# Optimization experiments

Measured on AMD Instinct MI355X. Metric: run time of the kernel, lower is better.

Reference implementation:

```python
import jax, jax.numpy as jnp
import numpy as np

EMB = 1024
B, N = 4, 2048


def setup_inputs() -> dict:
    key = jax.random.key(0)
    ks = jax.random.split(key, 10)
    s = 1.0 / np.sqrt(EMB)
    return {
        "x": jax.random.normal(ks[0], (B, N, EMB), dtype=jnp.float32),
        "Wq": jax.random.normal(ks[1], (EMB, EMB), dtype=jnp.float32) * s,
        "bq": jnp.zeros((EMB,), dtype=jnp.float32),
        "Wk": jax.random.normal(ks[2], (EMB, EMB), dtype=jnp.float32) * s,
        "bk": jnp.zeros((EMB,), dtype=jnp.float32),
        "Wv": jax.random.normal(ks[3], (EMB, EMB), dtype=jnp.float32) * s,
        "bv": jnp.zeros((EMB,), dtype=jnp.float32),
        "Wm": jax.random.normal(ks[4], (EMB, EMB), dtype=jnp.float32) * s,
        "bm": jnp.zeros((EMB,), dtype=jnp.float32),
    }


def reference(x, Wq, bq, Wk, bk, Wv, bv, Wm, bm):
    # Projections (torch Linear: x @ W^T + b; here W is stored pre-transposed)
    q = x @ Wq + bq  # [B,N,D]
    k = x @ Wk + bk
    v = x @ Wv + bv
    # scores[b,i,j] = q[b,i,:] . k[b,j,:]  (no 1/sqrt(d) scaling in original)
    scores = jnp.einsum("bid,bjd->bij", q, k)
    # NOTE: softmax over dim=1 (the query/i axis), as in the original
    alpha = jax.nn.softmax(scores, axis=1)  # [B,N,N]
    # t[b,j,d] = sum_i v[b,i,d] * alpha[b,i,j]  == alpha^T @ v per batch
    t = jnp.einsum("bij,bid->bjd", alpha, v)  # [B,N,D]
    # MLP(emb, emb, []) is a single Linear, followed by outer relu
    return jax.nn.relu(t @ Wm + bm)
```

## Files before the change

kernel.cpp:

```cpp
#include <hip/hip_runtime.h>
#include <hip/hip_bf16.h>
#include <hip/hip_fp16.h>
#include <math.h>

#define EMB 1024
#define SEQ 2048
#define BATCH 4

typedef _Float16 half8 __attribute__((ext_vector_type(8)));
typedef float floatx4 __attribute__((ext_vector_type(4)));

__device__ __forceinline__ void gload_lds16(const void* g, void* l) {
    __builtin_amdgcn_global_load_lds(
        (const __attribute__((address_space(1))) void*)g,
        (__attribute__((address_space(3))) void*)l, 16, 0, 0);
}

__device__ __forceinline__ void pipe_sync() {
    asm volatile("s_waitcnt vmcnt(0)" ::: "memory");
    __builtin_amdgcn_s_barrier();
    __builtin_amdgcn_sched_barrier(0);
}

template <int EPI>
__global__ __launch_bounds__(256) void gemm_bt(
    const _Float16* __restrict__ A, const _Float16* __restrict__ B,
    void* __restrict__ Cv, const float* __restrict__ bias,
    int M, int N, int K, long sAb, long sBb, long sCb) {
    __shared__ _Float16 As0[128 * 32];
    __shared__ _Float16 Bs0[128 * 32];
    __shared__ _Float16 As1[128 * 32];
    __shared__ _Float16 Bs1[128 * 32];
    const int tid = threadIdx.x;
    const int lane = tid & 63;
    const int wave = tid >> 6;
    const long zb = blockIdx.z;
    A += zb * sAb;
    B += zb * sBb;
    const int bm = blockIdx.x * 128;
    const int bn = blockIdx.y * 128;
    floatx4 acc[4][4];
#pragma unroll
    for (int mi = 0; mi < 4; ++mi)
#pragma unroll
        for (int ni = 0; ni < 4; ++ni) acc[mi][ni] = (floatx4){0.f, 0.f, 0.f, 0.f};

    const int srow = lane >> 2;
    const int scol = (lane & 3) * 8;
    const int wm = (wave >> 1) * 64;
    const int wn = (wave & 1) * 64;
    const int fr = lane & 15;
    const int fk = (lane >> 4) * 8;

#define STAGE(AS, BS, kt)                                                      \
    {                                                                          \
        _Pragma("unroll") for (int c = 0; c < 2; ++c) {                        \
            const int rr = wave * 32 + c * 16 + srow;                          \
            gload_lds16(A + (long)(bm + rr) * K + (kt) + scol,                 \
                        &AS[(wave * 2 + c) * 512]);                            \
            gload_lds16(B + (long)(bn + rr) * K + (kt) + scol,                 \
                        &BS[(wave * 2 + c) * 512]);                            \
        }                                                                      \
    }

#define COMPUTE(AS, BS)                                                        \
    {                                                                          \
        half8 af[4], bf[4];                                                    \
        _Pragma("unroll") for (int mi = 0; mi < 4; ++mi)                       \
            af[mi] = *(const half8*)&AS[(wm + mi * 16 + fr) * 32 + fk];        \
        _Pragma("unroll") for (int ni = 0; ni < 4; ++ni)                       \
            bf[ni] = *(const half8*)&BS[(wn + ni * 16 + fr) * 32 + fk];        \
        _Pragma("unroll") for (int mi = 0; mi < 4; ++mi)                       \
            _Pragma("unroll") for (int ni = 0; ni < 4; ++ni)                   \
                acc[mi][ni] = __builtin_amdgcn_mfma_f32_16x16x32_f16(          \
                    af[mi], bf[ni], acc[mi][ni], 0, 0, 0);                     \
    }

    const int T = K >> 5;
    STAGE(As0, Bs0, 0);
    pipe_sync();
    for (int t = 0; t < T; t += 2) {
        STAGE(As1, Bs1, (t + 1) << 5);
        COMPUTE(As0, Bs0);
        pipe_sync();
        if (t + 2 < T) STAGE(As0, Bs0, (t + 2) << 5);
        COMPUTE(As1, Bs1);
        pipe_sync();
    }
#undef STAGE
#undef COMPUTE

    const int er = (lane >> 4) * 4;
    const int ec = lane & 15;
#pragma unroll
    for (int mi = 0; mi < 4; ++mi) {
#pragma unroll
        for (int ni = 0; ni < 4; ++ni) {
            const int col = bn + wn + ni * 16 + ec;
#pragma unroll
            for (int r = 0; r < 4; ++r) {
                const int row = bm + wm + mi * 16 + er + r;
                float v = acc[mi][ni][r];
                if (EPI == 0 || EPI == 1 || EPI == 3) v += bias[col];
                if (EPI == 3) v = fmaxf(v, 0.f);
                if (EPI == 0 || EPI == 4) {
                    ((_Float16*)Cv)[zb * sCb + (long)row * N + col] = (_Float16)v;
                } else if (EPI == 1) {
                    const long b = row >> 11;
                    const long i = row & (SEQ - 1);
                    ((_Float16*)Cv)[(b * EMB + col) * SEQ + i] = (_Float16)v;
                } else {
                    ((float*)Cv)[zb * sCb + (long)row * N + col] = v;
                }
            }
        }
    }
}

__global__ __launch_bounds__(256) void softmax_rows(const float* __restrict__ P,
                                                    _Float16* __restrict__ Aout) {
    const long row = blockIdx.x;
    const float* p = P + row * (long)SEQ;
    const int tid = threadIdx.x;
    float4 x0 = ((const float4*)p)[2 * tid];
    float4 x1 = ((const float4*)p)[2 * tid + 1];
    float v[8] = {x0.x, x0.y, x0.z, x0.w, x1.x, x1.y, x1.z, x1.w};
    float m = v[0];
#pragma unroll
    for (int j = 1; j < 8; ++j) m = fmaxf(m, v[j]);
#pragma unroll
    for (int o = 32; o; o >>= 1) m = fmaxf(m, __shfl_xor(m, o));
    __shared__ float rbuf[4];
    __shared__ float sbuf[4];
    const int lane = tid & 63, wv = tid >> 6;
    if (!lane) rbuf[wv] = m;
    __syncthreads();
    m = fmaxf(fmaxf(rbuf[0], rbuf[1]), fmaxf(rbuf[2], rbuf[3]));
    float s = 0.f;
#pragma unroll
    for (int j = 0; j < 8; ++j) {
        v[j] = expf(v[j] - m);
        s += v[j];
    }
#pragma unroll
    for (int o = 32; o; o >>= 1) s += __shfl_xor(s, o);
    if (!lane) sbuf[wv] = s;
    __syncthreads();
    s = sbuf[0] + sbuf[1] + sbuf[2] + sbuf[3];
    const float inv = 1.f / s;
    half8 h;
#pragma unroll
    for (int j = 0; j < 8; ++j) h[j] = (_Float16)(v[j] * inv);
    *(half8*)(Aout + row * (long)SEQ + tid * 8) = h;
}

__global__ __launch_bounds__(256) void cast_x(const float* __restrict__ X,
                                              _Float16* __restrict__ Xh) {
    const long i = (long)(blockIdx.x * 256 + threadIdx.x) * 8;
    float4 a = ((const float4*)(X + i))[0];
    float4 b = ((const float4*)(X + i))[1];
    half8 h;
    h[0] = (_Float16)a.x; h[1] = (_Float16)a.y; h[2] = (_Float16)a.z; h[3] = (_Float16)a.w;
    h[4] = (_Float16)b.x; h[5] = (_Float16)b.y; h[6] = (_Float16)b.z; h[7] = (_Float16)b.w;
    *(half8*)(Xh + i) = h;
}

__global__ __launch_bounds__(256) void transpose_cast(const float* __restrict__ W,
                                                      _Float16* __restrict__ Wt) {
    __shared__ float tile[32][33];
    const int bx = blockIdx.x * 32;
    const int by = blockIdx.y * 32;
    const int tx = threadIdx.x, ty = threadIdx.y;
#pragma unroll
    for (int r = 0; r < 32; r += 8)
        tile[ty + r][tx] = W[(long)(by + ty + r) * EMB + bx + tx];
    __syncthreads();
#pragma unroll
    for (int r = 0; r < 32; r += 8)
        Wt[(long)(bx + ty + r) * EMB + by + tx] = (_Float16)tile[tx][ty + r];
}

extern "C" void kernel_launch(void* const* d_in, const int* in_sizes, int n_in,
                              void* d_out, int out_size, void* d_ws, size_t ws_size,
                              hipStream_t stream) {
    const float* x  = (const float*)d_in[0];
    const float* Wq = (const float*)d_in[1];
    const float* bq = (const float*)d_in[2];
    const float* Wk = (const float*)d_in[3];
    const float* bk = (const float*)d_in[4];
    const float* Wv = (const float*)d_in[5];
    const float* bv = (const float*)d_in[6];
    const float* Wm = (const float*)d_in[7];
    const float* bm = (const float*)d_in[8];
    float* out = (float*)d_out;

    char* ws = (char*)d_ws;
    const long MB = 1l << 20;
    _Float16* xh  = (_Float16*)(ws + 0 * MB);
    _Float16* wqt = (_Float16*)(ws + 16 * MB);
    _Float16* wkt = (_Float16*)(ws + 18 * MB);
    _Float16* wvt = (_Float16*)(ws + 20 * MB);
    _Float16* wmt = (_Float16*)(ws + 22 * MB);
    _Float16* q   = (_Float16*)(ws + 24 * MB);
    _Float16* k   = (_Float16*)(ws + 40 * MB);
    _Float16* vt  = (_Float16*)(ws + 56 * MB);
    _Float16* t   = (_Float16*)(ws + 72 * MB);
    float*    P   = (float*)(ws + 88 * MB);
    _Float16* al  = (_Float16*)(ws + 152 * MB);

    const long MN = (long)BATCH * SEQ;

    cast_x<<<4096, 256, 0, stream>>>(x, xh);
    transpose_cast<<<dim3(32, 32), dim3(32, 8), 0, stream>>>(Wq, wqt);
    transpose_cast<<<dim3(32, 32), dim3(32, 8), 0, stream>>>(Wk, wkt);
    transpose_cast<<<dim3(32, 32), dim3(32, 8), 0, stream>>>(Wv, wvt);
    transpose_cast<<<dim3(32, 32), dim3(32, 8), 0, stream>>>(Wm, wmt);

    gemm_bt<0><<<dim3(64, 8), 256, 0, stream>>>(xh, wqt, q, bq, (int)MN, EMB, EMB, 0, 0, 0);
    gemm_bt<0><<<dim3(64, 8), 256, 0, stream>>>(xh, wkt, k, bk, (int)MN, EMB, EMB, 0, 0, 0);
    gemm_bt<1><<<dim3(64, 8), 256, 0, stream>>>(xh, wvt, vt, bv, (int)MN, EMB, EMB, 0, 0, 0);

    gemm_bt<2><<<dim3(16, 16, BATCH), 256, 0, stream>>>(
        k, q, P, nullptr, SEQ, SEQ, EMB,
        (long)SEQ * EMB, (long)SEQ * EMB, (long)SEQ * SEQ);

    softmax_rows<<<BATCH * SEQ, 256, 0, stream>>>(P, al);

    gemm_bt<4><<<dim3(16, 8, BATCH), 256, 0, stream>>>(
        al, vt, t, nullptr, SEQ, EMB, SEQ,
        (long)SEQ * SEQ, (long)EMB * SEQ, (long)SEQ * EMB);

    gemm_bt<3><<<dim3(64, 8), 256, 0, stream>>>(t, wmt, out, bm, (int)MN, EMB, EMB, 0, 0, 0);
}
```

Measured before the change: 350.9 us.

## Use 256x128 tiles with 512 threads and a 4-stage LDS prefetch pipeline

Replaces the double-buffered 128x128 GEMM kernel with one using 512 threads, 256x128 block tiles and a 4-deep ring of LDS buffers. Three k-tiles are kept in flight, and partial vmcnt waits let later loads overlap the current MFMA work instead of draining all loads every step. Grid sizes are halved along M to match. The larger tile reuses each B tile more and hides memory latency better, at the cost of more LDS per block (96KB), which lowers occupancy, and fewer blocks for the smaller GEMMs.

```diff
diff --git a/kernel.cpp b/kernel.cpp
--- a/kernel.cpp
+++ b/kernel.cpp
@@ -16,28 +16,39 @@
         (__attribute__((address_space(3))) void*)l, 16, 0, 0);
 }
 
-__device__ __forceinline__ void pipe_sync() {
+__device__ __forceinline__ void bar_cnt6() {
+    __builtin_amdgcn_sched_barrier(0);
+    asm volatile("s_waitcnt vmcnt(6)" ::: "memory");
+    __builtin_amdgcn_s_barrier();
+    __builtin_amdgcn_sched_barrier(0);
+}
+__device__ __forceinline__ void bar_cnt3() {
+    __builtin_amdgcn_sched_barrier(0);
+    asm volatile("s_waitcnt vmcnt(3)" ::: "memory");
+    __builtin_amdgcn_s_barrier();
+    __builtin_amdgcn_sched_barrier(0);
+}
+__device__ __forceinline__ void bar_cnt0() {
+    __builtin_amdgcn_sched_barrier(0);
     asm volatile("s_waitcnt vmcnt(0)" ::: "memory");
     __builtin_amdgcn_s_barrier();
     __builtin_amdgcn_sched_barrier(0);
 }
 
 template <int EPI>
-__global__ __launch_bounds__(256) void gemm_bt(
+__global__ __launch_bounds__(512) void gemm_p(
     const _Float16* __restrict__ A, const _Float16* __restrict__ B,
     void* __restrict__ Cv, const float* __restrict__ bias,
     int M, int N, int K, long sAb, long sBb, long sCb) {
-    __shared__ _Float16 As0[128 * 32];
-    __shared__ _Float16 Bs0[128 * 32];
-    __shared__ _Float16 As1[128 * 32];
-    __shared__ _Float16 Bs1[128 * 32];
+    __shared__ _Float16 As[4][256 * 32];
+    __shared__ _Float16 Bs[4][128 * 32];
     const int tid = threadIdx.x;
     const int lane = tid & 63;
     const int wave = tid >> 6;
     const long zb = blockIdx.z;
     A += zb * sAb;
     B += zb * sBb;
-    const int bm = blockIdx.x * 128;
+    const int bm = blockIdx.x * 256;
     const int bn = blockIdx.y * 128;
     floatx4 acc[4][4];
 #pragma unroll
@@ -45,48 +56,54 @@
 #pragma unroll
         for (int ni = 0; ni < 4; ++ni) acc[mi][ni] = (floatx4){0.f, 0.f, 0.f, 0.f};
 
-    const int srow = lane >> 2;
-    const int scol = (lane & 3) * 8;
+    const int srow = tid >> 2;
+    const int scol = (tid & 3) * 8;
+    const long ag0 = (long)(bm + srow) * K + scol;
+    const long ag1 = (long)(bm + 128 + srow) * K + scol;
+    const long bg0 = (long)(bn + srow) * K + scol;
     const int wm = (wave >> 1) * 64;
     const int wn = (wave & 1) * 64;
     const int fr = lane & 15;
     const int fk = (lane >> 4) * 8;
 
-#define STAGE(AS, BS, kt)                                                      \
+#define STAGE(t_)                                                              \
     {                                                                          \
-        _Pragma("unroll") for (int c = 0; c < 2; ++c) {                        \
-            const int rr = wave * 32 + c * 16 + srow;                          \
-            gload_lds16(A + (long)(bm + rr) * K + (kt) + scol,                 \
-                        &AS[(wave * 2 + c) * 512]);                            \
-            gload_lds16(B + (long)(bn + rr) * K + (kt) + scol,                 \
-                        &BS[(wave * 2 + c) * 512]);                            \
-        }                                                                      \
-    }
-
-#define COMPUTE(AS, BS)                                                        \
+        const int b_ = (t_) & 3;                                               \
+        const int kt_ = (t_) * 32;                                             \
+        gload_lds16(A + ag0 + kt_, &As[b_][wave * 512]);                       \
+        gload_lds16(A + ag1 + kt_, &As[b_][4096 + wave * 512]);                \
+        gload_lds16(B + bg0 + kt_, &Bs[b_][wave * 512]);                       \
+    }
+
+#define COMPUTE(t_)                                                            \
     {                                                                          \
+        const int b_ = (t_) & 3;                                               \
         half8 af[4], bf[4];                                                    \
         _Pragma("unroll") for (int mi = 0; mi < 4; ++mi)                       \
-            af[mi] = *(const half8*)&AS[(wm + mi * 16 + fr) * 32 + fk];        \
+            af[mi] = *(const half8*)&As[b_][(wm + mi * 16 + fr) * 32 + fk];    \
         _Pragma("unroll") for (int ni = 0; ni < 4; ++ni)                       \
-            bf[ni] = *(const half8*)&BS[(wn + ni * 16 + fr) * 32 + fk];        \
+            bf[ni] = *(const half8*)&Bs[b_][(wn + ni * 16 + fr) * 32 + fk];    \
         _Pragma("unroll") for (int mi = 0; mi < 4; ++mi)                       \
             _Pragma("unroll") for (int ni = 0; ni < 4; ++ni)                   \
                 acc[mi][ni] = __builtin_amdgcn_mfma_f32_16x16x32_f16(          \
                     af[mi], bf[ni], acc[mi][ni], 0, 0, 0);                     \
     }
 
-    const int T = K >> 5;
-    STAGE(As0, Bs0, 0);
-    pipe_sync();
-    for (int t = 0; t < T; t += 2) {
-        STAGE(As1, Bs1, (t + 1) << 5);
-        COMPUTE(As0, Bs0);
-        pipe_sync();
-        if (t + 2 < T) STAGE(As0, Bs0, (t + 2) << 5);
-        COMPUTE(As1, Bs1);
-        pipe_sync();
-    }
+    const int NT = K >> 5;
+    STAGE(0);
+    STAGE(1);
+    STAGE(2);
+    bar_cnt6();
+    for (int t = 0; t < NT - 3; ++t) {
+        STAGE(t + 3);
+        COMPUTE(t);
+        bar_cnt6();
+    }
+    COMPUTE(NT - 3);
+    bar_cnt3();
+    COMPUTE(NT - 2);
+    bar_cnt0();
+    COMPUTE(NT - 1);
 #undef STAGE
 #undef COMPUTE
 
@@ -216,19 +233,19 @@
     transpose_cast<<<dim3(32, 32), dim3(32, 8), 0, stream>>>(Wv, wvt);
     transpose_cast<<<dim3(32, 32), dim3(32, 8), 0, stream>>>(Wm, wmt);
 
-    gemm_bt<0><<<dim3(64, 8), 256, 0, stream>>>(xh, wqt, q, bq, (int)MN, EMB, EMB, 0, 0, 0);
-    gemm_bt<0><<<dim3(64, 8), 256, 0, stream>>>(xh, wkt, k, bk, (int)MN, EMB, EMB, 0, 0, 0);
-    gemm_bt<1><<<dim3(64, 8), 256, 0, stream>>>(xh, wvt, vt, bv, (int)MN, EMB, EMB, 0, 0, 0);
-
-    gemm_bt<2><<<dim3(16, 16, BATCH), 256, 0, stream>>>(
+    gemm_p<0><<<dim3(32, 8), 512, 0, stream>>>(xh, wqt, q, bq, (int)MN, EMB, EMB, 0, 0, 0);
+    gemm_p<0><<<dim3(32, 8), 512, 0, stream>>>(xh, wkt, k, bk, (int)MN, EMB, EMB, 0, 0, 0);
+    gemm_p<1><<<dim3(32, 8), 512, 0, stream>>>(xh, wvt, vt, bv, (int)MN, EMB, EMB, 0, 0, 0);
+
+    gemm_p<2><<<dim3(8, 16, BATCH), 512, 0, stream>>>(
         k, q, P, nullptr, SEQ, SEQ, EMB,
         (long)SEQ * EMB, (long)SEQ * EMB, (long)SEQ * SEQ);
 
     softmax_rows<<<BATCH * SEQ, 256, 0, stream>>>(P, al);
 
-    gemm_bt<4><<<dim3(16, 8, BATCH), 256, 0, stream>>>(
+    gemm_p<4><<<dim3(8, 8, BATCH), 512, 0, stream>>>(
         al, vt, t, nullptr, SEQ, EMB, SEQ,
         (long)SEQ * SEQ, (long)EMB * SEQ, (long)SEQ * EMB);
 
-    gemm_bt<3><<<dim3(64, 8), 256, 0, stream>>>(t, wmt, out, bm, (int)MN, EMB, EMB, 0, 0, 0);
-}
+    gemm_p<3><<<dim3(32, 8), 512, 0, stream>>>(t, wmt, out, bm, (int)MN, EMB, EMB, 0, 0, 0);
+}
```

Result: slower. 373.3 us (+6.4%).

## Rewrite GEMM as 8-wave 256x128 tile with triple-buffered swizzled LDS pipeline

Applied to the files above, without the earlier changes.

The GEMM kernel moves from 4 waves on a 128x128 tile with BK=32 double buffering to 8 waves on a 256x128 tile with BK=64. LDS is triple-buffered and uses XOR-swizzled layouts to avoid bank conflicts. The loop is split into two phases per tile that interleave global-to-LDS loads with MFMA, using partial vmcnt waits and raised wave priority during compute. This aims to hide memory latency and raise MFMA utilization, at the cost of about 144KB of LDS per block (which limits occupancy) and fewer blocks per grid.

```diff
diff --git a/kernel.cpp b/kernel.cpp
--- a/kernel.cpp
+++ b/kernel.cpp
@@ -16,28 +16,25 @@
         (__attribute__((address_space(3))) void*)l, 16, 0, 0);
 }
 
-__device__ __forceinline__ void pipe_sync() {
-    asm volatile("s_waitcnt vmcnt(0)" ::: "memory");
+__device__ __forceinline__ void sbar() {
+    __builtin_amdgcn_sched_barrier(0);
     __builtin_amdgcn_s_barrier();
     __builtin_amdgcn_sched_barrier(0);
 }
 
 template <int EPI>
-__global__ __launch_bounds__(256) void gemm_bt(
+__global__ __launch_bounds__(512) void gemm_8p(
     const _Float16* __restrict__ A, const _Float16* __restrict__ B,
     void* __restrict__ Cv, const float* __restrict__ bias,
     int M, int N, int K, long sAb, long sBb, long sCb) {
-    __shared__ _Float16 As0[128 * 32];
-    __shared__ _Float16 Bs0[128 * 32];
-    __shared__ _Float16 As1[128 * 32];
-    __shared__ _Float16 Bs1[128 * 32];
+    __shared__ _Float16 lds[3 * 24576];
     const int tid = threadIdx.x;
     const int lane = tid & 63;
     const int wave = tid >> 6;
     const long zb = blockIdx.z;
     A += zb * sAb;
     B += zb * sBb;
-    const int bm = blockIdx.x * 128;
+    const int bm = blockIdx.x * 256;
     const int bn = blockIdx.y * 128;
     floatx4 acc[4][4];
 #pragma unroll
@@ -45,50 +42,85 @@
 #pragma unroll
         for (int ni = 0; ni < 4; ++ni) acc[mi][ni] = (floatx4){0.f, 0.f, 0.f, 0.f};
 
-    const int srow = lane >> 2;
-    const int scol = (lane & 3) * 8;
+    const int srow = tid >> 3;
+    const int ssl = (tid & 7) ^ (srow & 7);
+    const _Float16* Ag = A + (long)(bm + srow) * K + ssl * 8;
+    const _Float16* Bg = B + (long)(bn + srow) * K + ssl * 8;
+    const long K64 = (long)K * 64;
+    const int ldst = wave * 512;
+
     const int wm = (wave >> 1) * 64;
     const int wn = (wave & 1) * 64;
-    const int fr = lane & 15;
-    const int fk = (lane >> 4) * 8;
-
-#define STAGE(AS, BS, kt)                                                      \
-    {                                                                          \
-        _Pragma("unroll") for (int c = 0; c < 2; ++c) {                        \
-            const int rr = wave * 32 + c * 16 + srow;                          \
-            gload_lds16(A + (long)(bm + rr) * K + (kt) + scol,                 \
-                        &AS[(wave * 2 + c) * 512]);                            \
-            gload_lds16(B + (long)(bn + rr) * K + (kt) + scol,                 \
-                        &BS[(wave * 2 + c) * 512]);                            \
-        }                                                                      \
-    }
-
-#define COMPUTE(AS, BS)                                                        \
+    const int l15 = lane & 15;
+    const int x7 = lane & 7;
+    const int g4 = lane >> 4;
+    const int sl0 = (g4 ^ x7) * 8;
+    const int sl1 = ((4 + g4) ^ x7) * 8;
+    const int fA0 = (wm + l15) * 64 + sl0;
+    const int fA1 = (wm + l15) * 64 + sl1;
+    const int fB0 = 16384 + (wn + l15) * 64 + sl0;
+    const int fB1 = 16384 + (wn + l15) * 64 + sl1;
+
+#define STG_H0(kt_, so_)                                                       \
+    gload_lds16(Ag + (kt_), &lds[(so_) + ldst]);                               \
+    gload_lds16(Ag + K64 + (kt_), &lds[(so_) + 4096 + ldst]);                  \
+    gload_lds16(Bg + (kt_), &lds[(so_) + 16384 + ldst]);
+#define STG_H1(kt_, so_)                                                       \
+    gload_lds16(Ag + 2 * K64 + (kt_), &lds[(so_) + 8192 + ldst]);              \
+    gload_lds16(Ag + 3 * K64 + (kt_), &lds[(so_) + 12288 + ldst]);             \
+    gload_lds16(Bg + K64 + (kt_), &lds[(so_) + 16384 + 4096 + ldst]);
+
+#define PHASE(fa_, fb_, co_, STG_)                                             \
     {                                                                          \
         half8 af[4], bf[4];                                                    \
         _Pragma("unroll") for (int mi = 0; mi < 4; ++mi)                       \
-            af[mi] = *(const half8*)&AS[(wm + mi * 16 + fr) * 32 + fk];        \
+            af[mi] = *(const half8*)&lds[(co_) + (fa_) + mi * 1024];           \
         _Pragma("unroll") for (int ni = 0; ni < 4; ++ni)                       \
-            bf[ni] = *(const half8*)&BS[(wn + ni * 16 + fr) * 32 + fk];        \
+            bf[ni] = *(const half8*)&lds[(co_) + (fb_) + ni * 1024];           \
+        STG_                                                                   \
+        sbar();                                                                \
+        asm volatile("s_waitcnt lgkmcnt(0)" ::: "memory");                     \
+        __builtin_amdgcn_sched_barrier(0);                                     \
+        __builtin_amdgcn_s_setprio(1);                                         \
         _Pragma("unroll") for (int mi = 0; mi < 4; ++mi)                       \
             _Pragma("unroll") for (int ni = 0; ni < 4; ++ni)                   \
                 acc[mi][ni] = __builtin_amdgcn_mfma_f32_16x16x32_f16(          \
                     af[mi], bf[ni], acc[mi][ni], 0, 0, 0);                     \
-    }
-
-    const int T = K >> 5;
-    STAGE(As0, Bs0, 0);
-    pipe_sync();
-    for (int t = 0; t < T; t += 2) {
-        STAGE(As1, Bs1, (t + 1) << 5);
-        COMPUTE(As0, Bs0);
-        pipe_sync();
-        if (t + 2 < T) STAGE(As0, Bs0, (t + 2) << 5);
-        COMPUTE(As1, Bs1);
-        pipe_sync();
-    }
-#undef STAGE
-#undef COMPUTE
+        __builtin_amdgcn_s_setprio(0);                                         \
+    }
+
+#define TILE_END(n_)                                                           \
+    __builtin_amdgcn_sched_barrier(0);                                         \
+    asm volatile("s_waitcnt vmcnt(" #n_ ")" ::: "memory");                     \
+    __builtin_amdgcn_s_barrier();                                              \
+    __builtin_amdgcn_sched_barrier(0);
+
+    STG_H0(0, 0) STG_H1(0, 0)
+    STG_H0(64, 24576) STG_H1(64, 24576)
+    TILE_END(6)
+    int co = 0, so = 49152;
+    const int NT = K >> 6;
+    for (int t = 0; t < NT - 2; ++t) {
+        const long kt2 = (long)(t + 2) << 6;
+        PHASE(fA0, fB0, co, STG_H0(kt2, so))
+        sbar();
+        PHASE(fA1, fB1, co, STG_H1(kt2, so))
+        TILE_END(6)
+        co += 24576; if (co == 73728) co = 0;
+        so += 24576; if (so == 73728) so = 0;
+    }
+    PHASE(fA0, fB0, co, )
+    sbar();
+    PHASE(fA1, fB1, co, )
+    TILE_END(0)
+    co += 24576; if (co == 73728) co = 0;
+    PHASE(fA0, fB0, co, )
+    sbar();
+    PHASE(fA1, fB1, co, )
+#undef STG_H0
+#undef STG_H1
+#undef PHASE
+#undef TILE_END
 
     const int er = (lane >> 4) * 4;
     const int ec = lane & 15;
@@ -216,19 +248,19 @@
     transpose_cast<<<dim3(32, 32), dim3(32, 8), 0, stream>>>(Wv, wvt);
     transpose_cast<<<dim3(32, 32), dim3(32, 8), 0, stream>>>(Wm, wmt);
 
-    gemm_bt<0><<<dim3(64, 8), 256, 0, stream>>>(xh, wqt, q, bq, (int)MN, EMB, EMB, 0, 0, 0);
-    gemm_bt<0><<<dim3(64, 8), 256, 0, stream>>>(xh, wkt, k, bk, (int)MN, EMB, EMB, 0, 0, 0);
-    gemm_bt<1><<<dim3(64, 8), 256, 0, stream>>>(xh, wvt, vt, bv, (int)MN, EMB, EMB, 0, 0, 0);
-
-    gemm_bt<2><<<dim3(16, 16, BATCH), 256, 0, stream>>>(
+    gemm_8p<0><<<dim3(32, 8), 512, 0, stream>>>(xh, wqt, q, bq, (int)MN, EMB, EMB, 0, 0, 0);
+    gemm_8p<0><<<dim3(32, 8), 512, 0, stream>>>(xh, wkt, k, bk, (int)MN, EMB, EMB, 0, 0, 0);
+    gemm_8p<1><<<dim3(32, 8), 512, 0, stream>>>(xh, wvt, vt, bv, (int)MN, EMB, EMB, 0, 0, 0);
+
+    gemm_8p<2><<<dim3(8, 16, BATCH), 512, 0, stream>>>(
         k, q, P, nullptr, SEQ, SEQ, EMB,
         (long)SEQ * EMB, (long)SEQ * EMB, (long)SEQ * SEQ);
 
     softmax_rows<<<BATCH * SEQ, 256, 0, stream>>>(P, al);
 
-    gemm_bt<4><<<dim3(16, 8, BATCH), 256, 0, stream>>>(
+    gemm_8p<4><<<dim3(8, 8, BATCH), 512, 0, stream>>>(
         al, vt, t, nullptr, SEQ, EMB, SEQ,
         (long)SEQ * SEQ, (long)EMB * SEQ, (long)SEQ * EMB);
 
-    gemm_bt<3><<<dim3(64, 8), 256, 0, stream>>>(t, wmt, out, bm, (int)MN, EMB, EMB, 0, 0, 0);
-}
+    gemm_8p<3><<<dim3(32, 8), 512, 0, stream>>>(t, wmt, out, bm, (int)MN, EMB, EMB, 0, 0, 0);
+}
```

Result: faster. 303.3 us (-13.6%).
